# Optimization experiments

Measured on AMD Instinct MI355X. Metric: run time of the kernel, lower is better.

The kernel has to match this reference:

```python
import jax, jax.numpy as jnp
from jax import lax
import numpy as np

LAMBDA_DAG = 0.5
B, C = 64, 5000
PARENT_PROB = 0.0008  # ~4 parents per GO term


def setup_inputs() -> dict:
    key = jax.random.key(0)
    k1, k2, k3 = jax.random.split(key, 3)
    logits = jax.random.normal(k1, (B, C), dtype=jnp.float32)
    # sparse multilabel targets (binary floats, like GO annotations)
    labels = (jax.random.uniform(k2, (B, C)) < 0.02).astype(jnp.float32)
    # sparse binary DAG adjacency: dag[i, j] = 1 if j is a parent of i
    dag = (jax.random.uniform(k3, (C, C)) < PARENT_PROB).astype(jnp.float32)
    dag = dag * (1.0 - jnp.eye(C, dtype=jnp.float32))  # no self-parents
    return {"logits": logits, "labels": labels, "dag_matrix": dag}


def reference(logits, labels, dag_matrix):
    # BCEWithLogitsLoss (mean): log(1 + exp(l)) - l * y, numerically stable
    bce = jnp.mean(jnp.logaddexp(0.0, logits) - logits * labels)

    probs = jax.nn.sigmoid(logits)                      # [B, C]
    mask = (dag_matrix > 0).astype(probs.dtype)          # [C, C]
    n_par = mask.sum(axis=1)                             # [C] parents per child

    # Accumulate sum over batch of relu(p_child - p_parent)^2 as a [C, C] matrix
    # via scan over the batch dim (keeps peak memory at one [C, C] tile).
    def body(acc, p):  # p: [C]
        d = jnp.maximum(p[:, None] - p[None, :], 0.0)
        return acc + d * d, None

    nterms = probs.shape[1]
    viol_sum, _ = lax.scan(body, jnp.zeros((nterms, nterms), probs.dtype), probs)

    # per-child-term mean over (batch, n_parents_i), only for terms with parents
    per_term = (viol_sum * mask).sum(axis=1)             # [C]
    batch = jnp.asarray(probs.shape[0], probs.dtype)
    term_mean = jnp.where(n_par > 0, per_term / (batch * jnp.maximum(n_par, 1.0)), 0.0)

    total_edges = mask.sum()
    dag_penalty = jnp.where(total_edges > 0, term_mean.sum() / jnp.maximum(total_edges, 1.0), 0.0)

    loss = bce + LAMBDA_DAG * dag_penalty
    return loss
```

## Files before the change

### kernel.cpp

```cpp
#include <hip/hip_runtime.h>
#include <math.h>

#define LAMBDA_DAG 0.5f

__global__ void __launch_bounds__(256) k_probs_bce(
        const float* __restrict__ logits,
        const float* __restrict__ labels,
        float* __restrict__ pT,
        float* __restrict__ bce_part,
        float* __restrict__ per_term,
        float* __restrict__ npar,
        int B, int C) {
    const int nb  = gridDim.x * gridDim.y;
    const int bid = blockIdx.y * gridDim.x + blockIdx.x;

    for (int i = bid * blockDim.x + threadIdx.x; i < C; i += nb * blockDim.x) {
        per_term[i] = 0.f;
        npar[i] = 0.f;
    }

    __shared__ float tile[64][17];
    __shared__ float sred[256];

    const int c0 = blockIdx.x * 64;
    const int b0 = blockIdx.y * 16;
    const int rows = (B - b0 < 16) ? (B - b0) : 16;

    const int lc = threadIdx.x & 63;
    const int c  = c0 + lc;
    const bool valid = (c < C);
    float acc = 0.f;

    if (rows > 0) {
        for (int r = threadIdx.x >> 6; r < rows; r += (blockDim.x >> 6)) {
            const int b = b0 + r;
            float l = 0.f, y = 0.f;
            if (valid) {
                l = logits[(size_t)b * C + c];
                y = labels[(size_t)b * C + c];
                acc += fmaxf(l, 0.f) + log1pf(expf(-fabsf(l))) - l * y;
            }
            tile[lc][r] = 1.f / (1.f + expf(-l));
        }
    }
    __syncthreads();

    if (rows > 0) {
        if ((rows & 3) == 0) {
            const int r4  = rows >> 2;
            const int tot = 64 * r4;
            for (int t = threadIdx.x; t < tot; t += blockDim.x) {
                const int row = t / r4;
                const int q   = t - row * r4;
                const int c2  = c0 + row;
                if (c2 < C) {
                    float4 v;
                    v.x = tile[row][q * 4 + 0];
                    v.y = tile[row][q * 4 + 1];
                    v.z = tile[row][q * 4 + 2];
                    v.w = tile[row][q * 4 + 3];
                    *(float4*)(pT + (size_t)c2 * B + b0 + q * 4) = v;
                }
            }
        } else {
            const int tot = 64 * rows;
            for (int t = threadIdx.x; t < tot; t += blockDim.x) {
                const int row = t / rows;
                const int r   = t - row * rows;
                const int c2  = c0 + row;
                if (c2 < C) pT[(size_t)c2 * B + b0 + r] = tile[row][r];
            }
        }
    }

    sred[threadIdx.x] = acc;
    __syncthreads();
    for (int s = blockDim.x >> 1; s > 0; s >>= 1) {
        if (threadIdx.x < s) sred[threadIdx.x] += sred[threadIdx.x + s];
        __syncthreads();
    }
    if (threadIdx.x == 0) bce_part[bid] = sred[0];
}

#define SCAN_U 8
__global__ void __launch_bounds__(256) k_dag_scan(
        const float* __restrict__ dag,
        const float* __restrict__ pT,
        float* __restrict__ per_term,
        float* __restrict__ npar,
        int B, int C) {
    const int N  = C * C;
    const int N4 = N >> 2;
    const float4* dag4 = (const float4*)dag;
    const int tileN   = blockDim.x * SCAN_U;
    const int gstride = gridDim.x * tileN;
    const int B4 = B >> 2;
    const bool b4ok = ((B & 3) == 0);

    for (int base = blockIdx.x * tileN + threadIdx.x; base < N4;
         base += gstride) {
        float4 d[SCAN_U];
#pragma unroll
        for (int u = 0; u < SCAN_U; ++u) {
            const int idx = base + u * 256;
            if (idx < N4) d[u] = dag4[idx];
            else          d[u] = make_float4(0.f, 0.f, 0.f, 0.f);
        }
        unsigned any = 0u;
#pragma unroll
        for (int u = 0; u < SCAN_U; ++u) {
            any |= __float_as_uint(d[u].x) | __float_as_uint(d[u].y) |
                   __float_as_uint(d[u].z) | __float_as_uint(d[u].w);
        }
        if (any != 0u) {
#pragma unroll
            for (int u = 0; u < SCAN_U; ++u) {
                const float dv[4] = {d[u].x, d[u].y, d[u].z, d[u].w};
#pragma unroll
                for (int k = 0; k < 4; ++k) {
                    if (dv[k] > 0.f) {
                        const int e = (base + u * 256) * 4 + k;
                        const int i = e / C;
                        const int j = e - i * C;
                        float s = 0.f;
                        if (b4ok) {
                            const float4* pi4 = (const float4*)(pT + (size_t)i * B);
                            const float4* pj4 = (const float4*)(pT + (size_t)j * B);
#pragma unroll 2
                            for (int t = 0; t < B4; ++t) {
                                float4 a = pi4[t], b = pj4[t];
                                float d0 = fmaxf(a.x - b.x, 0.f);
                                float d1 = fmaxf(a.y - b.y, 0.f);
                                float d2 = fmaxf(a.z - b.z, 0.f);
                                float d3 = fmaxf(a.w - b.w, 0.f);
                                s += d0 * d0 + d1 * d1 + d2 * d2 + d3 * d3;
                            }
                        } else {
                            for (int b = 0; b < B; ++b) {
                                float diff = fmaxf(pT[(size_t)i * B + b] -
                                                   pT[(size_t)j * B + b], 0.f);
                                s += diff * diff;
                            }
                        }
                        atomicAdd(&per_term[i], s);
                        atomicAdd(&npar[i], 1.f);
                    }
                }
            }
        }
    }
}

__global__ void k_final(const float* __restrict__ per_term,
                        const float* __restrict__ npar,
                        const float* __restrict__ bce_part, int nb,
                        float* __restrict__ out, int B, int C) {
    float bs = 0.f, ps = 0.f, es = 0.f;
    for (int k = threadIdx.x; k < nb; k += blockDim.x) bs += bce_part[k];
    for (int i = threadIdx.x; i < C; i += blockDim.x) {
        float np = npar[i];
        es += np;
        if (np > 0.f) ps += per_term[i] / ((float)B * np);
    }
    __shared__ float s1[256], s2[256], s3[256];
    s1[threadIdx.x] = bs;
    s2[threadIdx.x] = ps;
    s3[threadIdx.x] = es;
    __syncthreads();
    for (int s = blockDim.x >> 1; s > 0; s >>= 1) {
        if (threadIdx.x < s) {
            s1[threadIdx.x] += s1[threadIdx.x + s];
            s2[threadIdx.x] += s2[threadIdx.x + s];
            s3[threadIdx.x] += s3[threadIdx.x + s];
        }
        __syncthreads();
    }
    if (threadIdx.x == 0) {
        float penalty = (s3[0] > 0.f) ? (s2[0] / s3[0]) : 0.f;
        out[0] = s1[0] / (float)(B * C) + LAMBDA_DAG * penalty;
    }
}

extern "C" void kernel_launch(void* const* d_in, const int* in_sizes, int n_in,
                              void* d_out, int out_size, void* d_ws, size_t ws_size,
                              hipStream_t stream) {
    const float* logits = (const float*)d_in[0];
    const float* labels = (const float*)d_in[1];
    const float* dag    = (const float*)d_in[2];
    float* out = (float*)d_out;

    const int C = (int)(sqrt((double)in_sizes[2]) + 0.5);
    const int B = in_sizes[0] / C;

    float* ws       = (float*)d_ws;
    float* pT       = ws;
    float* per_term = pT + (size_t)C * B;
    float* nparw    = per_term + C;
    float* bce_part = nparw + C;

    const int gridAx = (C + 63) / 64;
    const int gridAy = (B + 15) / 16;
    dim3 gA(gridAx, gridAy);
    k_probs_bce<<<gA, 256, 0, stream>>>(logits, labels, pT, bce_part,
                                        per_term, nparw, B, C);

    const int N4 = (C * C) >> 2;
    const int tileN = 256 * SCAN_U;
    const int gridB = (N4 + tileN - 1) / tileN;
    k_dag_scan<<<gridB, 256, 0, stream>>>(dag, pT, per_term, nparw, B, C);

    k_final<<<1, 256, 0, stream>>>(per_term, nparw, bce_part, gridAx * gridAy,
                                   out, B, C);
}
```

Before: 190.5 us.

## Compact DAG edges into a list, then process edges wave-parallel

Splits the DAG scan into two passes. The first streams the dense adjacency, collects nonzero edge indices into a shared-memory buffer and appends them to a global edge list. A second kernel then gives each edge to one 64-lane wave, which computes the batch reduction with a shuffle reduction. This removes the serial per-thread 64-element dot loop and the divergence it causes in the streaming pass, at the cost of an extra launch, atomics on shared and global counters, and workspace for the list.

```diff
diff --git a/kernel.cpp b/kernel.cpp
--- a/kernel.cpp
+++ b/kernel.cpp
@@ -2,6 +2,8 @@
 #include <math.h>
 
 #define LAMBDA_DAG 0.5f
+#define SCAN_U 8
+#define LBUF_CAP 2048
 
 __global__ void __launch_bounds__(256) k_probs_bce(
         const float* __restrict__ logits,
@@ -10,10 +12,12 @@
         float* __restrict__ bce_part,
         float* __restrict__ per_term,
         float* __restrict__ npar,
+        int* __restrict__ ecnt,
         int B, int C) {
     const int nb  = gridDim.x * gridDim.y;
     const int bid = blockIdx.y * gridDim.x + blockIdx.x;
 
+    if (bid == 0 && threadIdx.x == 0) *ecnt = 0;
     for (int i = bid * blockDim.x + threadIdx.x; i < C; i += nb * blockDim.x) {
         per_term[i] = 0.f;
         npar[i] = 0.f;
@@ -82,30 +86,46 @@
     if (threadIdx.x == 0) bce_part[bid] = sred[0];
 }
 
-#define SCAN_U 8
-__global__ void __launch_bounds__(256) k_dag_scan(
+__device__ __forceinline__ void process_edge_inline(
+        unsigned e, const float* __restrict__ pT,
+        float* __restrict__ per_term, float* __restrict__ npar, int B, int C) {
+    const int i = (int)(e / (unsigned)C);
+    const int j = (int)(e - (unsigned)i * (unsigned)C);
+    float s = 0.f;
+    for (int b = 0; b < B; ++b) {
+        float df = fmaxf(pT[(size_t)i * B + b] - pT[(size_t)j * B + b], 0.f);
+        s += df * df;
+    }
+    atomicAdd(&per_term[i], s);
+    atomicAdd(&npar[i], 1.f);
+}
+
+__global__ void __launch_bounds__(256) k_dag_compact(
         const float* __restrict__ dag,
         const float* __restrict__ pT,
         float* __restrict__ per_term,
         float* __restrict__ npar,
+        unsigned* __restrict__ elist,
+        int* __restrict__ ecnt,
+        int elist_cap,
         int B, int C) {
+    __shared__ unsigned lbuf[LBUF_CAP];
+    __shared__ int lcnt;
+    __shared__ int gbase;
+    if (threadIdx.x == 0) lcnt = 0;
+    __syncthreads();
+
     const int N  = C * C;
     const int N4 = N >> 2;
     const float4* dag4 = (const float4*)dag;
-    const int tileN   = blockDim.x * SCAN_U;
-    const int gstride = gridDim.x * tileN;
-    const int B4 = B >> 2;
-    const bool b4ok = ((B & 3) == 0);
-
-    for (int base = blockIdx.x * tileN + threadIdx.x; base < N4;
-         base += gstride) {
+    const int tileN = 256 * SCAN_U;
+    const int NT = N4 / tileN;
+
+    for (int t = blockIdx.x; t < NT; t += gridDim.x) {
+        const int base = t * tileN + threadIdx.x;
         float4 d[SCAN_U];
 #pragma unroll
-        for (int u = 0; u < SCAN_U; ++u) {
-            const int idx = base + u * 256;
-            if (idx < N4) d[u] = dag4[idx];
-            else          d[u] = make_float4(0.f, 0.f, 0.f, 0.f);
-        }
+        for (int u = 0; u < SCAN_U; ++u) d[u] = dag4[base + u * 256];
         unsigned any = 0u;
 #pragma unroll
         for (int u = 0; u < SCAN_U; ++u) {
@@ -119,34 +139,85 @@
 #pragma unroll
                 for (int k = 0; k < 4; ++k) {
                     if (dv[k] > 0.f) {
-                        const int e = (base + u * 256) * 4 + k;
-                        const int i = e / C;
-                        const int j = e - i * C;
-                        float s = 0.f;
-                        if (b4ok) {
-                            const float4* pi4 = (const float4*)(pT + (size_t)i * B);
-                            const float4* pj4 = (const float4*)(pT + (size_t)j * B);
-#pragma unroll 2
-                            for (int t = 0; t < B4; ++t) {
-                                float4 a = pi4[t], b = pj4[t];
-                                float d0 = fmaxf(a.x - b.x, 0.f);
-                                float d1 = fmaxf(a.y - b.y, 0.f);
-                                float d2 = fmaxf(a.z - b.z, 0.f);
-                                float d3 = fmaxf(a.w - b.w, 0.f);
-                                s += d0 * d0 + d1 * d1 + d2 * d2 + d3 * d3;
-                            }
-                        } else {
-                            for (int b = 0; b < B; ++b) {
-                                float diff = fmaxf(pT[(size_t)i * B + b] -
-                                                   pT[(size_t)j * B + b], 0.f);
-                                s += diff * diff;
-                            }
-                        }
-                        atomicAdd(&per_term[i], s);
-                        atomicAdd(&npar[i], 1.f);
+                        const unsigned e = (unsigned)((base + u * 256) * 4 + k);
+                        const int pos = atomicAdd(&lcnt, 1);
+                        if (pos < LBUF_CAP) lbuf[pos] = e;
+                        else process_edge_inline(e, pT, per_term, npar, B, C);
                     }
                 }
             }
+        }
+    }
+
+    for (int q = NT * tileN + blockIdx.x * blockDim.x + threadIdx.x; q < N4;
+         q += gridDim.x * blockDim.x) {
+        float4 d = dag4[q];
+        const float dv[4] = {d.x, d.y, d.z, d.w};
+#pragma unroll
+        for (int k = 0; k < 4; ++k) {
+            if (dv[k] > 0.f) {
+                const unsigned e = (unsigned)(q * 4 + k);
+                const int pos = atomicAdd(&lcnt, 1);
+                if (pos < LBUF_CAP) lbuf[pos] = e;
+                else process_edge_inline(e, pT, per_term, npar, B, C);
+            }
+        }
+    }
+    for (int e = (N4 << 2) + blockIdx.x * blockDim.x + threadIdx.x; e < N;
+         e += gridDim.x * blockDim.x) {
+        if (dag[e] > 0.f) {
+            const int pos = atomicAdd(&lcnt, 1);
+            if (pos < LBUF_CAP) lbuf[pos] = (unsigned)e;
+            else process_edge_inline((unsigned)e, pT, per_term, npar, B, C);
+        }
+    }
+
+    __syncthreads();
+    if (threadIdx.x == 0) {
+        int n = (lcnt < LBUF_CAP) ? lcnt : LBUF_CAP;
+        gbase = atomicAdd(ecnt, n);
+        lcnt = n;
+    }
+    __syncthreads();
+    const int n = lcnt;
+    const int gb = gbase;
+    for (int t = threadIdx.x; t < n; t += blockDim.x) {
+        const int gpos = gb + t;
+        if (gpos < elist_cap) elist[gpos] = lbuf[t];
+        else process_edge_inline(lbuf[t], pT, per_term, npar, B, C);
+    }
+}
+
+__global__ void __launch_bounds__(256) k_edges(
+        const float* __restrict__ pT,
+        const unsigned* __restrict__ elist,
+        const int* __restrict__ ecnt,
+        int elist_cap,
+        float* __restrict__ per_term,
+        float* __restrict__ npar,
+        int B, int C) {
+    int n = *ecnt;
+    if (n > elist_cap) n = elist_cap;
+    const int lane = threadIdx.x & 63;
+    const int wid  = (blockIdx.x * blockDim.x + threadIdx.x) >> 6;
+    const int nw   = (gridDim.x * blockDim.x) >> 6;
+
+    for (int t = wid; t < n; t += nw) {
+        const unsigned e = elist[t];
+        const int i = (int)(e / (unsigned)C);
+        const int j = (int)(e - (unsigned)i * (unsigned)C);
+        const float* pi = pT + (size_t)i * B;
+        const float* pj = pT + (size_t)j * B;
+        float s = 0.f;
+        for (int b = lane; b < B; b += 64) {
+            float df = fmaxf(pi[b] - pj[b], 0.f);
+            s += df * df;
+        }
+#pragma unroll
+        for (int off = 32; off > 0; off >>= 1) s += __shfl_down(s, off, 64);
+        if (lane == 0) {
+            atomicAdd(&per_term[i], s);
+            atomicAdd(&npar[i], 1.f);
         }
     }
 }
@@ -192,23 +263,33 @@
     const int C = (int)(sqrt((double)in_sizes[2]) + 0.5);
     const int B = in_sizes[0] / C;
 
+    const int gridAx = (C + 63) / 64;
+    const int gridAy = (B + 15) / 16;
+    const int nbA = gridAx * gridAy;
+
     float* ws       = (float*)d_ws;
     float* pT       = ws;
     float* per_term = pT + (size_t)C * B;
     float* nparw    = per_term + C;
     float* bce_part = nparw + C;
-
-    const int gridAx = (C + 63) / 64;
-    const int gridAy = (B + 15) / 16;
+    int*   ecnt     = (int*)(bce_part + nbA);
+    unsigned* elist = (unsigned*)(ecnt + 1);
+
+    size_t used_words = (size_t)C * B + 2 * (size_t)C + nbA + 1;
+    size_t total_words = ws_size / 4;
+    long long capll = (long long)total_words - (long long)used_words;
+    int elist_cap = (capll < 0) ? 0
+                  : (capll > 0x7fffffff ? 0x7fffffff : (int)capll);
+
     dim3 gA(gridAx, gridAy);
     k_probs_bce<<<gA, 256, 0, stream>>>(logits, labels, pT, bce_part,
-                                        per_term, nparw, B, C);
-
-    const int N4 = (C * C) >> 2;
-    const int tileN = 256 * SCAN_U;
-    const int gridB = (N4 + tileN - 1) / tileN;
-    k_dag_scan<<<gridB, 256, 0, stream>>>(dag, pT, per_term, nparw, B, C);
-
-    k_final<<<1, 256, 0, stream>>>(per_term, nparw, bce_part, gridAx * gridAy,
-                                   out, B, C);
-}
+                                        per_term, nparw, ecnt, B, C);
+
+    k_dag_compact<<<2048, 256, 0, stream>>>(dag, pT, per_term, nparw,
+                                            elist, ecnt, elist_cap, B, C);
+
+    k_edges<<<512, 256, 0, stream>>>(pT, elist, ecnt, elist_cap,
+                                     per_term, nparw, B, C);
+
+    k_final<<<1, 256, 0, stream>>>(per_term, nparw, bce_part, nbA, out, B, C);
+}
```

Result: no change. 191.3 us (+0.4%).

## Fuse probs with DAG scan, compact edges to list, process edges wavefront-parallel

Applied to the files above, without the earlier changes.

Merges the probability/BCE computation into the DAG scan launch, so the scan blocks stream the dense 100MB adjacency concurrently with the probs blocks. Nonzero edges go into per-block edge lists, staged through shared memory, instead of being processed inline. A separate kernel then evaluates each edge with a full wavefront reduction over the batch. The scan also adds register double-buffered prefetch and nontemporal loads for half the matrix. This splits the scan across two launches and adds workspace-size-dependent fallback paths, which raises complexity and risks breakage if the workspace is small.

```diff
diff --git a/kernel.cpp b/kernel.cpp
--- a/kernel.cpp
+++ b/kernel.cpp
@@ -2,150 +2,242 @@
 #include <math.h>
 
 #define LAMBDA_DAG 0.5f
-
-__global__ void __launch_bounds__(256) k_probs_bce(
+#define SCAN_U 8
+#define TILEN (256 * SCAN_U)
+#define LBUF_CAP 2048
+
+typedef float f4v __attribute__((ext_vector_type(4)));
+
+__device__ __forceinline__ void process_edge_inline(
+        unsigned e, const float* __restrict__ pT,
+        float* __restrict__ per_term, float* __restrict__ npar, int B, int C) {
+    const unsigned ui = e / (unsigned)C;
+    const int i = (int)ui;
+    const int j = (int)(e - ui * (unsigned)C);
+    float s = 0.f;
+    for (int b = 0; b < B; ++b) {
+        float df = fmaxf(pT[(size_t)i * B + b] - pT[(size_t)j * B + b], 0.f);
+        s += df * df;
+    }
+    atomicAdd(&per_term[i], s);
+    atomicAdd(&npar[i], 1.f);
+}
+
+template <int USE_NT>
+__device__ __forceinline__ f4v ld4(const float* p) {
+#if defined(__HIP_DEVICE_COMPILE__)
+    if constexpr (USE_NT) return __builtin_nontemporal_load((const f4v*)p);
+#endif
+    return *(const f4v*)p;
+}
+
+#define PUSH_EDGE(E)                                                        \
+    {                                                                       \
+        const int pos = atomicAdd(&lcnt, 1);                                \
+        if (pos < LBUF_CAP) lbuf[pos] = (E);                                \
+        else if (pos < segw) seg[pos] = (E);                                \
+        else if (inline_ok) process_edge_inline((E), pT, per_term, npar,    \
+                                                B, C);                      \
+    }
+
+#define PROCESS_TILE(R, tbase)                                              \
+    {                                                                       \
+        unsigned any = 0u;                                                  \
+        _Pragma("unroll")                                                   \
+        for (int u = 0; u < SCAN_U; ++u)                                    \
+            any |= __float_as_uint(R[u][0]) | __float_as_uint(R[u][1]) |    \
+                   __float_as_uint(R[u][2]) | __float_as_uint(R[u][3]);     \
+        if (any != 0u) {                                                    \
+            _Pragma("unroll")                                               \
+            for (int u = 0; u < SCAN_U; ++u) {                              \
+                _Pragma("unroll")                                           \
+                for (int k = 0; k < 4; ++k) {                               \
+                    if (R[u][k] > 0.f) {                                    \
+                        const unsigned e = (unsigned)(((tbase) + u * 256 +  \
+                                           (int)threadIdx.x) * 4 + k);      \
+                        PUSH_EDGE(e);                                       \
+                    }                                                       \
+                }                                                           \
+            }                                                               \
+        }                                                                   \
+    }
+
+template <int USE_NT>
+__global__ void __launch_bounds__(256) k_main(
         const float* __restrict__ logits,
         const float* __restrict__ labels,
+        const float* __restrict__ dag,
         float* __restrict__ pT,
         float* __restrict__ bce_part,
         float* __restrict__ per_term,
         float* __restrict__ npar,
-        int B, int C) {
-    const int nb  = gridDim.x * gridDim.y;
-    const int bid = blockIdx.y * gridDim.x + blockIdx.x;
-
-    for (int i = bid * blockDim.x + threadIdx.x; i < C; i += nb * blockDim.x) {
-        per_term[i] = 0.f;
-        npar[i] = 0.f;
-    }
+        unsigned* __restrict__ elist,
+        int* __restrict__ bcount,
+        int segw, int inline_ok,
+        int tb, int te,
+        int sb_base, int sbN,
+        int do_tails,
+        int nbAx, int nbAy, int B, int C) {
+    const int nbA = nbAx * nbAy;
+    const int bid = blockIdx.x;
+    const int tid = threadIdx.x;
 
     __shared__ float tile[64][17];
     __shared__ float sred[256];
-
-    const int c0 = blockIdx.x * 64;
-    const int b0 = blockIdx.y * 16;
-    const int rows = (B - b0 < 16) ? (B - b0) : 16;
-
-    const int lc = threadIdx.x & 63;
-    const int c  = c0 + lc;
-    const bool valid = (c < C);
-    float acc = 0.f;
-
-    if (rows > 0) {
-        for (int r = threadIdx.x >> 6; r < rows; r += (blockDim.x >> 6)) {
-            const int b = b0 + r;
-            float l = 0.f, y = 0.f;
-            if (valid) {
-                l = logits[(size_t)b * C + c];
-                y = labels[(size_t)b * C + c];
-                acc += fmaxf(l, 0.f) + log1pf(expf(-fabsf(l))) - l * y;
-            }
-            tile[lc][r] = 1.f / (1.f + expf(-l));
-        }
-    }
+    __shared__ unsigned lbuf[LBUF_CAP];
+    __shared__ int lcnt;
+
+    if (bid < nbA) {
+        for (int i = bid * 256 + tid; i < C; i += nbA * 256) {
+            per_term[i] = 0.f;
+            npar[i] = 0.f;
+        }
+        const int bx = bid % nbAx, by = bid / nbAx;
+        const int c0 = bx * 64;
+        const int b0 = by * 16;
+        const int rows = (B - b0 < 16) ? (B - b0) : 16;
+        const int lc = tid & 63;
+        const int c  = c0 + lc;
+        const bool valid = (c < C);
+        float acc = 0.f;
+        if (rows > 0) {
+            for (int r = tid >> 6; r < rows; r += 4) {
+                const int b = b0 + r;
+                float l = 0.f, y = 0.f;
+                if (valid) {
+                    l = logits[(size_t)b * C + c];
+                    y = labels[(size_t)b * C + c];
+                    acc += fmaxf(l, 0.f) + log1pf(expf(-fabsf(l))) - l * y;
+                }
+                tile[lc][r] = 1.f / (1.f + expf(-l));
+            }
+        }
+        __syncthreads();
+        if (rows > 0) {
+            if ((rows & 3) == 0) {
+                const int r4 = rows >> 2;
+                const int tot = 64 * r4;
+                for (int t = tid; t < tot; t += 256) {
+                    const int row = t / r4;
+                    const int q = t - row * r4;
+                    const int c2 = c0 + row;
+                    if (c2 < C) {
+                        float4 v;
+                        v.x = tile[row][q * 4 + 0];
+                        v.y = tile[row][q * 4 + 1];
+                        v.z = tile[row][q * 4 + 2];
+                        v.w = tile[row][q * 4 + 3];
+                        *(float4*)(pT + (size_t)c2 * B + b0 + q * 4) = v;
+                    }
+                }
+            } else {
+                const int tot = 64 * rows;
+                for (int t = tid; t < tot; t += 256) {
+                    const int row = t / rows;
+                    const int r = t - row * rows;
+                    const int c2 = c0 + row;
+                    if (c2 < C) pT[(size_t)c2 * B + b0 + r] = tile[row][r];
+                }
+            }
+        }
+        sred[tid] = acc;
+        __syncthreads();
+        for (int s = 128; s > 0; s >>= 1) {
+            if (tid < s) sred[tid] += sred[tid + s];
+            __syncthreads();
+        }
+        if (tid == 0) bce_part[bid] = sred[0];
+        return;
+    }
+
+    const int lsb = bid - nbA;
+    const int sb  = sb_base + lsb;
+    if (tid == 0) lcnt = 0;
     __syncthreads();
-
-    if (rows > 0) {
-        if ((rows & 3) == 0) {
-            const int r4  = rows >> 2;
-            const int tot = 64 * r4;
-            for (int t = threadIdx.x; t < tot; t += blockDim.x) {
-                const int row = t / r4;
-                const int q   = t - row * r4;
-                const int c2  = c0 + row;
-                if (c2 < C) {
-                    float4 v;
-                    v.x = tile[row][q * 4 + 0];
-                    v.y = tile[row][q * 4 + 1];
-                    v.z = tile[row][q * 4 + 2];
-                    v.w = tile[row][q * 4 + 3];
-                    *(float4*)(pT + (size_t)c2 * B + b0 + q * 4) = v;
+    unsigned* __restrict__ seg = elist + (size_t)sb * (size_t)segw;
+
+    const int N  = C * C;
+    const int N4 = N >> 2;
+    const int NT = N4 / TILEN;
+    const int span = (te > tb) ? ((te - tb) + sbN - 1) / sbN : 0;
+    const int t0 = tb + lsb * span;
+    const int t1 = (t0 + span < te) ? (t0 + span) : te;
+
+    if (t0 < t1) {
+        const float* p = dag + ((size_t)t0 * TILEN + tid) * 4;
+        f4v a[SCAN_U], b[SCAN_U];
+#pragma unroll
+        for (int u = 0; u < SCAN_U; ++u) a[u] = ld4<USE_NT>(p + u * 1024);
+        for (int t = t0; t < t1; ++t) {
+            const bool last = (t + 1 == t1);
+            if (!last) {
+#pragma unroll
+                for (int u = 0; u < SCAN_U; ++u)
+                    b[u] = ld4<USE_NT>(p + TILEN * 4 + u * 1024);
+            }
+            PROCESS_TILE(a, t * TILEN);
+            if (!last) {
+#pragma unroll
+                for (int u = 0; u < SCAN_U; ++u) a[u] = b[u];
+            }
+            p += TILEN * 4;
+        }
+    }
+
+    if (do_tails) {
+        for (int q = NT * TILEN + lsb * 256 + tid; q < N4; q += sbN * 256) {
+            f4v d = ld4<0>(dag + (size_t)q * 4);
+#pragma unroll
+            for (int k = 0; k < 4; ++k) {
+                if (d[k] > 0.f) {
+                    const unsigned e = (unsigned)(q * 4 + k);
+                    PUSH_EDGE(e);
                 }
             }
-        } else {
-            const int tot = 64 * rows;
-            for (int t = threadIdx.x; t < tot; t += blockDim.x) {
-                const int row = t / rows;
-                const int r   = t - row * rows;
-                const int c2  = c0 + row;
-                if (c2 < C) pT[(size_t)c2 * B + b0 + r] = tile[row][r];
-            }
-        }
-    }
-
-    sred[threadIdx.x] = acc;
+        }
+        for (int e = (N4 << 2) + lsb * 256 + tid; e < N; e += sbN * 256) {
+            if (dag[e] > 0.f) PUSH_EDGE((unsigned)e);
+        }
+    }
+
     __syncthreads();
-    for (int s = blockDim.x >> 1; s > 0; s >>= 1) {
-        if (threadIdx.x < s) sred[threadIdx.x] += sred[threadIdx.x + s];
-        __syncthreads();
-    }
-    if (threadIdx.x == 0) bce_part[bid] = sred[0];
-}
-
-#define SCAN_U 8
-__global__ void __launch_bounds__(256) k_dag_scan(
-        const float* __restrict__ dag,
+    const int n  = lcnt;
+    const int nl = (n < LBUF_CAP) ? n : LBUF_CAP;
+    for (int t = tid; t < nl; t += 256)
+        if (t < segw) seg[t] = lbuf[t];
+    if (tid == 0) bcount[sb] = (n < segw) ? n : segw;
+}
+
+__global__ void __launch_bounds__(256) k_edges(
         const float* __restrict__ pT,
+        const unsigned* __restrict__ elist,
+        const int* __restrict__ bcount, int segw, int nseg,
         float* __restrict__ per_term,
         float* __restrict__ npar,
         int B, int C) {
-    const int N  = C * C;
-    const int N4 = N >> 2;
-    const float4* dag4 = (const float4*)dag;
-    const int tileN   = blockDim.x * SCAN_U;
-    const int gstride = gridDim.x * tileN;
-    const int B4 = B >> 2;
-    const bool b4ok = ((B & 3) == 0);
-
-    for (int base = blockIdx.x * tileN + threadIdx.x; base < N4;
-         base += gstride) {
-        float4 d[SCAN_U];
-#pragma unroll
-        for (int u = 0; u < SCAN_U; ++u) {
-            const int idx = base + u * 256;
-            if (idx < N4) d[u] = dag4[idx];
-            else          d[u] = make_float4(0.f, 0.f, 0.f, 0.f);
-        }
-        unsigned any = 0u;
-#pragma unroll
-        for (int u = 0; u < SCAN_U; ++u) {
-            any |= __float_as_uint(d[u].x) | __float_as_uint(d[u].y) |
-                   __float_as_uint(d[u].z) | __float_as_uint(d[u].w);
-        }
-        if (any != 0u) {
-#pragma unroll
-            for (int u = 0; u < SCAN_U; ++u) {
-                const float dv[4] = {d[u].x, d[u].y, d[u].z, d[u].w};
-#pragma unroll
-                for (int k = 0; k < 4; ++k) {
-                    if (dv[k] > 0.f) {
-                        const int e = (base + u * 256) * 4 + k;
-                        const int i = e / C;
-                        const int j = e - i * C;
-                        float s = 0.f;
-                        if (b4ok) {
-                            const float4* pi4 = (const float4*)(pT + (size_t)i * B);
-                            const float4* pj4 = (const float4*)(pT + (size_t)j * B);
-#pragma unroll 2
-                            for (int t = 0; t < B4; ++t) {
-                                float4 a = pi4[t], b = pj4[t];
-                                float d0 = fmaxf(a.x - b.x, 0.f);
-                                float d1 = fmaxf(a.y - b.y, 0.f);
-                                float d2 = fmaxf(a.z - b.z, 0.f);
-                                float d3 = fmaxf(a.w - b.w, 0.f);
-                                s += d0 * d0 + d1 * d1 + d2 * d2 + d3 * d3;
-                            }
-                        } else {
-                            for (int b = 0; b < B; ++b) {
-                                float diff = fmaxf(pT[(size_t)i * B + b] -
-                                                   pT[(size_t)j * B + b], 0.f);
-                                s += diff * diff;
-                            }
-                        }
-                        atomicAdd(&per_term[i], s);
-                        atomicAdd(&npar[i], 1.f);
-                    }
-                }
+    const int lane = threadIdx.x & 63;
+    const int w    = threadIdx.x >> 6;
+    for (int sb = blockIdx.x; sb < nseg; sb += gridDim.x) {
+        int n = bcount[sb];
+        if (n > segw) n = segw;
+        const unsigned* seg = elist + (size_t)sb * (size_t)segw;
+        for (int t = w; t < n; t += 4) {
+            const unsigned e = seg[t];
+            const unsigned ui = e / (unsigned)C;
+            const int i = (int)ui;
+            const int j = (int)(e - ui * (unsigned)C);
+            const float* pi = pT + (size_t)i * B;
+            const float* pj = pT + (size_t)j * B;
+            float s = 0.f;
+            for (int b = lane; b < B; b += 64) {
+                float df = fmaxf(pi[b] - pj[b], 0.f);
+                s += df * df;
+            }
+#pragma unroll
+            for (int off = 32; off > 0; off >>= 1) s += __shfl_down(s, off, 64);
+            if (lane == 0) {
+                atomicAdd(&per_term[i], s);
+                atomicAdd(&npar[i], 1.f);
             }
         }
     }
@@ -192,23 +284,69 @@
     const int C = (int)(sqrt((double)in_sizes[2]) + 0.5);
     const int B = in_sizes[0] / C;
 
+    const int gridAx = (C + 63) / 64;
+    const int gridAy = (B + 15) / 16;
+    const int nbA = gridAx * gridAy;
+
+    const int N4 = (C * C) >> 2;
+    const int NT = N4 / TILEN;
+    const int scanBa = 1024, scanBb = 1024;
+    const int nseg = scanBa + scanBb;
+    const int NTa = NT / 2;
+    const int spanA = (NTa > 0) ? (NTa + scanBa - 1) / scanBa : 0;
+    const int spanB = ((NT - NTa) + scanBb - 1) / scanBb;
+    const int spanM = (spanA > spanB) ? spanA : spanB;
+    const long long segw_full = (long long)(spanM + 1) * TILEN * 4;
+
     float* ws       = (float*)d_ws;
     float* pT       = ws;
     float* per_term = pT + (size_t)C * B;
     float* nparw    = per_term + C;
     float* bce_part = nparw + C;
-
-    const int gridAx = (C + 63) / 64;
-    const int gridAy = (B + 15) / 16;
-    dim3 gA(gridAx, gridAy);
-    k_probs_bce<<<gA, 256, 0, stream>>>(logits, labels, pT, bce_part,
-                                        per_term, nparw, B, C);
-
-    const int N4 = (C * C) >> 2;
-    const int tileN = 256 * SCAN_U;
-    const int gridB = (N4 + tileN - 1) / tileN;
-    k_dag_scan<<<gridB, 256, 0, stream>>>(dag, pT, per_term, nparw, B, C);
-
-    k_final<<<1, 256, 0, stream>>>(per_term, nparw, bce_part, gridAx * gridAy,
-                                   out, B, C);
-}
+    int*   bcount   = (int*)(bce_part + nbA);
+    unsigned* elist = (unsigned*)(bcount + nseg);
+
+    const size_t base_words = (size_t)C * B + 2 * (size_t)C + nbA + nseg;
+    const size_t ws_words = ws_size / 4;
+    long long avail = (ws_words > base_words)
+                    ? (long long)(ws_words - base_words) : 0;
+
+    int fused, inline_ok, segw;
+    if (avail >= segw_full * nseg) {
+        fused = 1; inline_ok = 0;
+        segw = (int)segw_full;
+    } else {
+        fused = 0; inline_ok = 1;
+        long long sw = avail / nseg;
+        if (sw > 0x7fffffffLL) sw = 0x7fffffffLL;
+        segw = (int)(sw < 0 ? 0 : sw);
+    }
+
+    if (fused) {
+        k_main<1><<<nbA + scanBa, 256, 0, stream>>>(
+            logits, labels, dag, pT, bce_part, per_term, nparw,
+            elist, bcount, segw, 0,
+            0, NTa, 0, scanBa, 0, gridAx, gridAy, B, C);
+        k_main<0><<<scanBb, 256, 0, stream>>>(
+            logits, labels, dag, pT, bce_part, per_term, nparw,
+            elist, bcount, segw, 0,
+            NTa, NT, scanBa, scanBb, 1, 0, 0, B, C);
+    } else {
+        k_main<0><<<nbA, 256, 0, stream>>>(
+            logits, labels, dag, pT, bce_part, per_term, nparw,
+            elist, bcount, segw, 0,
+            0, 0, 0, 1, 0, gridAx, gridAy, B, C);
+        k_main<1><<<scanBa, 256, 0, stream>>>(
+            logits, labels, dag, pT, bce_part, per_term, nparw,
+            elist, bcount, segw, inline_ok,
+            0, NTa, 0, scanBa, 0, 0, 0, B, C);
+        k_main<0><<<scanBb, 256, 0, stream>>>(
+            logits, labels, dag, pT, bce_part, per_term, nparw,
+            elist, bcount, segw, inline_ok,
+            NTa, NT, scanBa, scanBb, 1, 0, 0, B, C);
+    }
+
+    k_edges<<<nseg, 256, 0, stream>>>(pT, elist, bcount, segw, nseg,
+                                      per_term, nparw, B, C);
+    k_final<<<1, 256, 0, stream>>>(per_term, nparw, bce_part, nbA, out, B, C);
+}
```

Result: faster. 171.8 us (-9.8%).
